# Performance work log

Measured on AMD Instinct MI355X. Metric: run time of the kernel, lower is better.

The kernel has to match this reference:

```python
import jax, jax.numpy as jnp
import numpy as np

# BERT-base dims; 768 and max_sent_num=64 come from the module/config.
N, S, V, D, L, H, F = 8, 512, 30522, 768, 12, 12, 3072
DH = D // H
MAX_SENT = 64
LN_EPS = 1e-12
SCALE = float(np.sqrt(DH))


def _ln(x, g, b):
    m = jnp.mean(x, axis=-1, keepdims=True)
    v = jnp.mean(jnp.square(x - m), axis=-1, keepdims=True)
    return (x - m) * jax.lax.rsqrt(v + LN_EPS) * g + b


def setup_inputs() -> dict:
    key = jax.random.key(0)
    ks = jax.random.split(key, 10)
    # random token ids in a range avoiding the special ids 102/103
    ids = jax.random.randint(ks[0], (N, S), 999, 30000, dtype=jnp.int32)
    # variable per-doc sentence region -> ragged number of [MASK](103) separators (8..64)
    cutoff = jax.random.randint(ks[1], (N, 1), 64, S + 1)
    pos = jnp.arange(S)[None, :]
    sent_pos = ((pos % 8) == 7) & (pos < cutoff)
    ids = jnp.where(sent_pos, 103, ids)
    ids = ids.at[:, 0].set(102)  # exactly one [SEP]=102 per doc (required by the slice-assign)
    amask = jnp.ones((N, S), dtype=jnp.int32)
    g = lambda k, shape: 0.02 * jax.random.normal(k, shape, dtype=jnp.float32)
    inp = dict(input_ids_bert=ids, attention_mask_bert=amask)
    inp["tok_emb"] = g(ks[2], (V, D))
    inp["pos_emb"] = g(ks[3], (S, D))
    inp["emb_ln_g"] = jnp.ones((D,), jnp.float32)
    inp["emb_ln_b"] = jnp.zeros((D,), jnp.float32)
    inp["Wqkv"] = g(ks[4], (L, D, 3 * D))
    inp["bqkv"] = jnp.zeros((L, 3 * D), jnp.float32)
    inp["Wo"] = g(ks[5], (L, D, D))
    inp["bo"] = jnp.zeros((L, D), jnp.float32)
    inp["ln1_g"] = jnp.ones((L, D), jnp.float32)
    inp["ln1_b"] = jnp.zeros((L, D), jnp.float32)
    inp["W1"] = g(ks[6], (L, D, F))
    inp["b1"] = jnp.zeros((L, F), jnp.float32)
    inp["W2"] = g(ks[7], (L, F, D))
    inp["b2"] = jnp.zeros((L, D), jnp.float32)
    inp["ln2_g"] = jnp.ones((L, D), jnp.float32)
    inp["ln2_b"] = jnp.zeros((L, D), jnp.float32)
    return inp


def _bert(ids, amask, tok_emb, pos_emb, emb_ln_g, emb_ln_b,
          Wqkv, bqkv, Wo, bo, ln1_g, ln1_b, W1, b1, W2, b2, ln2_g, ln2_b):
    x = tok_emb[ids] + pos_emb[None, :, :]            # [N,S,D]
    x = _ln(x, emb_ln_g, emb_ln_b)
    bias = (1.0 - amask[:, None, None, :].astype(x.dtype)) * -1e9  # [N,1,1,S]

    def layer(x, p):
        wqkv, bq, wo, bo_, g1, b1n, w1, b1f, w2, b2f, g2, b2n = p
        qkv = x @ wqkv + bq
        q, k, v = jnp.split(qkv, 3, axis=-1)
        q = q.reshape(N, S, H, DH)
        k = k.reshape(N, S, H, DH)
        v = v.reshape(N, S, H, DH)
        att = jnp.einsum('bqhd,bkhd->bhqk', q, k) / SCALE + bias
        att = jax.nn.softmax(att, axis=-1)
        o = jnp.einsum('bhqk,bkhd->bqhd', att, v).reshape(N, S, D)
        x2 = _ln(x + o @ wo + bo_, g1, b1n)
        h = jax.nn.gelu(x2 @ w1 + b1f, approximate=False)
        return _ln(x2 + h @ w2 + b2f, g2, b2n), None

    x, _ = jax.lax.scan(layer, x, (Wqkv, bqkv, Wo, bo, ln1_g, ln1_b, W1, b1, W2, b2, ln2_g, ln2_b))
    return x


def _gather_scatter(ids, h):
    # Vectorized form of the per-doc python loop:
    #   out[doc, :n_sent] = concat([cls_emb(102), sent_embs(103)])[:-1]
    mask_sent = ids == 103
    mask_cls = ids == 102
    n_cls = mask_cls.sum(axis=1, keepdims=True)              # == 1 per doc
    total_sent = mask_sent.sum(axis=1, keepdims=True)        # ragged count
    rank_sent = jnp.cumsum(mask_sent, axis=1) - 1
    rank_cls = jnp.cumsum(mask_cls, axis=1) - 1
    dest = jnp.where(mask_cls, rank_cls,
                     jnp.where(mask_sent, n_cls + rank_sent, MAX_SENT))
    valid = (mask_cls | mask_sent) & (dest < total_sent) & (dest < MAX_SENT)
    dest_safe = jnp.where(valid, dest, MAX_SENT)             # dump invalid into scratch row
    vals = jnp.where(valid[..., None], h, 0.0)
    out = jnp.zeros((ids.shape[0], MAX_SENT + 1, D), dtype=h.dtype)
    out = out.at[jnp.arange(ids.shape[0])[:, None], dest_safe].set(vals)
    return out[:, :MAX_SENT]


def reference(input_ids_bert, attention_mask_bert, tok_emb, pos_emb, emb_ln_g, emb_ln_b,
              Wqkv, bqkv, Wo, bo, ln1_g, ln1_b, W1, b1, W2, b2, ln2_g, ln2_b):
    h = _bert(input_ids_bert, attention_mask_bert, tok_emb, pos_emb, emb_ln_g, emb_ln_b,
              Wqkv, bqkv, Wo, bo, ln1_g, ln1_b, W1, b1, W2, b2, ln2_g, ln2_b)
    return _gather_scatter(input_ids_bert, h)
```

## Files before the change

### kernel.cpp

```cpp
#include <hip/hip_runtime.h>
#include <hip/hip_bf16.h>

#define DEV static __device__ __forceinline__

using short8 = __attribute__((ext_vector_type(8))) short;
using f32x4 = __attribute__((ext_vector_type(4))) float;

DEV short f2bf(float f) {
  union { float f; unsigned u; } x; x.f = f;
  unsigned r = x.u + 0x7fffu + ((x.u >> 16) & 1u);
  return (short)(r >> 16);
}

DEV float bf2f(short s) {
  union { unsigned u; float f; } x; x.u = ((unsigned)(unsigned short)s) << 16;
  return x.f;
}

DEV void gload16(const void* g, void* lds) {
  __builtin_amdgcn_global_load_lds(
      (const __attribute__((address_space(1))) void*)g,
      (__attribute__((address_space(3))) void*)lds, 16, 0, 0);
}

DEV float erf_fast(float x) {
  float ax = fabsf(x);
  float t = __fdividef(1.f, 1.f + 0.3275911f * ax);
  float y = t * (0.254829592f + t * (-0.284496736f +
            t * (1.421413741f + t * (-1.453152027f + t * 1.061405429f))));
  float r = 1.f - y * __expf(-ax * ax);
  return copysignf(r, x);
}

DEV void swz_grid(int& bx, int& by, int& bz) {
  const int nx = gridDim.x, ny = gridDim.y;
  const int nwg = nx * ny * (int)gridDim.z;
  const int lin = (int)blockIdx.x + nx * ((int)blockIdx.y + ny * (int)blockIdx.z);
  const int cpx = nwg >> 3;
  const int s = (lin & 7) * cpx + (lin >> 3);
  bx = s % nx;
  const int t = s / nx;
  by = t % ny;
  bz = t / ny;
}

DEV void transpose_tile(const float* in, short* out, int K, int N, int tt, int nt,
                        int tid, short (*t)[72]) {
  const int n0 = (tt % nt) * 64, k0 = (tt / nt) * 64;
  #pragma unroll
  for (int p = 0; p < 4; ++p) {
    int r = p * 16 + (tid >> 4), c4 = tid & 15;
    float4 v = *reinterpret_cast<const float4*>(in + (size_t)(k0 + r) * N + n0 + c4 * 4);
    t[r][c4 * 4 + 0] = f2bf(v.x);
    t[r][c4 * 4 + 1] = f2bf(v.y);
    t[r][c4 * 4 + 2] = f2bf(v.z);
    t[r][c4 * 4 + 3] = f2bf(v.w);
  }
  __syncthreads();
  #pragma unroll
  for (int q = 0; q < 2; ++q) {
    int n = tid >> 2, kc = (tid & 3) + q * 4;
    short8 o;
    #pragma unroll
    for (int j = 0; j < 8; ++j) o[j] = t[kc * 8 + j][n];
    *reinterpret_cast<short8*>(out + (size_t)(n0 + n) * K + k0 + kc * 8) = o;
  }
}

__global__ __launch_bounds__(256) void transpose_all_k(
    const float* __restrict__ Wqkv, const float* __restrict__ Wo,
    const float* __restrict__ W1, const float* __restrict__ W2,
    short* __restrict__ wqkvT, short* __restrict__ woT,
    short* __restrict__ w1T, short* __restrict__ w2T)
{
  __shared__ short t[64][72];
  const int b = blockIdx.x, tid = threadIdx.x;
  const float* in; short* out; int K, N, tt, nt;
  if (b < 432)       { in = Wqkv; out = wqkvT; K = 768;  N = 2304; tt = b;        nt = 36; }
  else if (b < 576)  { in = Wo;   out = woT;   K = 768;  N = 768;  tt = b - 432;  nt = 12; }
  else if (b < 1152) { in = W1;   out = w1T;   K = 768;  N = 3072; tt = b - 576;  nt = 48; }
  else               { in = W2;   out = w2T;   K = 3072; N = 768;  tt = b - 1152; nt = 12; }
  transpose_tile(in, out, K, N, tt, nt, tid, t);
}

__global__ __launch_bounds__(256) void transpose12_k(
    const float* __restrict__ Wqkv, const float* __restrict__ Wo,
    const float* __restrict__ W1, const float* __restrict__ W2,
    short* __restrict__ wqkvT, short* __restrict__ woT,
    short* __restrict__ w1T, short* __restrict__ w2T)
{
  __shared__ short t[64][72];
  const int b = blockIdx.x, l = blockIdx.z, tid = threadIdx.x;
  const float* in; short* out; int K, N, tt, nt;
  if (b < 432)       { in = Wqkv + (size_t)l * 768 * 2304; out = wqkvT + (size_t)l * 2304 * 768; K = 768;  N = 2304; tt = b;        nt = 36; }
  else if (b < 576)  { in = Wo   + (size_t)l * 768 * 768;  out = woT   + (size_t)l * 768 * 768;  K = 768;  N = 768;  tt = b - 432;  nt = 12; }
  else if (b < 1152) { in = W1   + (size_t)l * 768 * 3072; out = w1T   + (size_t)l * 3072 * 768; K = 768;  N = 3072; tt = b - 576;  nt = 48; }
  else               { in = W2   + (size_t)l * 3072 * 768; out = w2T   + (size_t)l * 768 * 3072; K = 3072; N = 768;  tt = b - 1152; nt = 12; }
  transpose_tile(in, out, K, N, tt, nt, tid, t);
}

template <int BM, int EPI>
__global__ __launch_bounds__(256) void gemm_bt(
    const short* __restrict__ A, const short* __restrict__ Bt,
    const float* __restrict__ bias, const float* __restrict__ resid,
    void* __restrict__ Cout, int M, int Nn, int K)
{
  constexpr int AW = BM / 64;
  constexpr int MI = BM / 32;
  __shared__ short As[2 * BM * 32];
  __shared__ short Bs[2 * 128 * 32];
  int bx, by, bz;
  swz_grid(bx, by, bz);
  const int tid = threadIdx.x, lane = tid & 63, w = tid >> 6;
  const int wr = w >> 1, wc = w & 1;
  const int l15 = lane & 15, l4 = lane >> 4;
  const int m0 = by * BM, n0 = bx * 128;
  const int crow = lane >> 2, ccol = (lane & 3) * 8;

  f32x4 acc[MI][4] = {};

  for (int k0 = 0; k0 < K; k0 += 64) {
    #pragma unroll
    for (int ks = 0; ks < 2; ++ks) {
      #pragma unroll
      for (int s = 0; s < AW; ++s) {
        int c = w * AW + s;
        gload16(A + (size_t)(m0 + c * 16 + crow) * K + k0 + ks * 32 + ccol,
                &As[ks * BM * 32 + c * 512]);
      }
      #pragma unroll
      for (int s = 0; s < 2; ++s) {
        int c = w * 2 + s;
        gload16(Bt + (size_t)(n0 + c * 16 + crow) * K + k0 + ks * 32 + ccol,
                &Bs[ks * 128 * 32 + c * 512]);
      }
    }
    __syncthreads();

    #pragma unroll
    for (int ks = 0; ks < 2; ++ks) {
      short8 af[MI], bfr[4];
      #pragma unroll
      for (int i = 0; i < MI; ++i)
        af[i] = *reinterpret_cast<const short8*>(
            &As[ks * BM * 32 + (wr * (BM / 2) + i * 16 + l15) * 32 + l4 * 8]);
      #pragma unroll
      for (int j = 0; j < 4; ++j)
        bfr[j] = *reinterpret_cast<const short8*>(
            &Bs[ks * 128 * 32 + (wc * 64 + j * 16 + l15) * 32 + l4 * 8]);
      #pragma unroll
      for (int i = 0; i < MI; ++i)
        #pragma unroll
        for (int j = 0; j < 4; ++j)
          acc[i][j] = __builtin_amdgcn_mfma_f32_16x16x32_bf16(af[i], bfr[j], acc[i][j], 0, 0, 0);
    }
    __syncthreads();
  }

  #pragma unroll
  for (int i = 0; i < MI; ++i) {
    #pragma unroll
    for (int j = 0; j < 4; ++j) {
      #pragma unroll
      for (int r = 0; r < 4; ++r) {
        int row = m0 + wr * (BM / 2) + i * 16 + l4 * 4 + r;
        int col = n0 + wc * 64 + j * 16 + l15;
        float v = acc[i][j][r] + bias[col];
        if constexpr (EPI == 1) v = 0.5f * v * (1.0f + erf_fast(v * 0.70710678118654752f));
        ((short*)Cout)[(size_t)row * Nn + col] = f2bf(v);
      }
    }
  }
}

__global__ __launch_bounds__(256) void gemm_sk(
    const short* __restrict__ A, const short* __restrict__ Bt,
    short* __restrict__ p0, short* __restrict__ p1,
    short* __restrict__ p2, short* __restrict__ p3,
    int M, int Nn, int Kstride, int Klen)
{
  __shared__ short As[2 * 128 * 32];
  __shared__ short Bs[2 * 128 * 32];
  int bx, by, bz;
  swz_grid(bx, by, bz);
  const int tid = threadIdx.x, lane = tid & 63, w = tid >> 6;
  const int wr = w >> 1, wc = w & 1;
  const int l15 = lane & 15, l4 = lane >> 4;
  const int m0 = by * 128, n0 = bx * 128;
  const int koff = bz * Klen;
  const int crow = lane >> 2, ccol = (lane & 3) * 8;

  f32x4 acc[4][4] = {};

  for (int k0 = 0; k0 < Klen; k0 += 64) {
    #pragma unroll
    for (int ks = 0; ks < 2; ++ks) {
      #pragma unroll
      for (int s = 0; s < 2; ++s) {
        int c = w * 2 + s;
        gload16(A + (size_t)(m0 + c * 16 + crow) * Kstride + koff + k0 + ks * 32 + ccol,
                &As[ks * 4096 + c * 512]);
      }
      #pragma unroll
      for (int s = 0; s < 2; ++s) {
        int c = w * 2 + s;
        gload16(Bt + (size_t)(n0 + c * 16 + crow) * Kstride + koff + k0 + ks * 32 + ccol,
                &Bs[ks * 4096 + c * 512]);
      }
    }
    __syncthreads();

    #pragma unroll
    for (int ks = 0; ks < 2; ++ks) {
      short8 af[4], bfr[4];
      #pragma unroll
      for (int i = 0; i < 4; ++i)
        af[i] = *reinterpret_cast<const short8*>(
            &As[ks * 4096 + (wr * 64 + i * 16 + l15) * 32 + l4 * 8]);
      #pragma unroll
      for (int j = 0; j < 4; ++j)
        bfr[j] = *reinterpret_cast<const short8*>(
            &Bs[ks * 4096 + (wc * 64 + j * 16 + l15) * 32 + l4 * 8]);
      #pragma unroll
      for (int i = 0; i < 4; ++i)
        #pragma unroll
        for (int j = 0; j < 4; ++j)
          acc[i][j] = __builtin_amdgcn_mfma_f32_16x16x32_bf16(af[i], bfr[j], acc[i][j], 0, 0, 0);
    }
    __syncthreads();
  }

  short* P = (bz == 0) ? p0 : (bz == 1) ? p1 : (bz == 2) ? p2 : p3;
  #pragma unroll
  for (int i = 0; i < 4; ++i)
    #pragma unroll
    for (int j = 0; j < 4; ++j)
      #pragma unroll
      for (int r = 0; r < 4; ++r) {
        int row = m0 + wr * 64 + i * 16 + l4 * 4 + r;
        int col = n0 + wc * 64 + j * 16 + l15;
        P[(size_t)row * Nn + col] = f2bf(acc[i][j][r]);
      }
}

__global__ __launch_bounds__(256) void attn_k(
    const short* __restrict__ qkv, const int* __restrict__ amask,
    short* __restrict__ out)
{
  __shared__ short Kl[64][72];
  __shared__ short Vt[64][68];
  __shared__ short Pl[4][16][72];
  int bx, by, bz;
  swz_grid(bx, by, bz);
  const int b = bz, h = by, qt = bx;
  const int tid = threadIdx.x, lane = tid & 63, w = tid >> 6;
  const int l15 = lane & 15, l4 = lane >> 4;
  const int tok0 = b * 512;
  const int q0 = qt * 64 + w * 16;

  short8 qf[2];
  #pragma unroll
  for (int kk = 0; kk < 2; ++kk)
    qf[kk] = *reinterpret_cast<const short8*>(
        qkv + (size_t)(tok0 + q0 + l15) * 2304 + h * 64 + kk * 32 + l4 * 8);

  f32x4 oacc[4] = {};
  float mrow[4], lrow[4];
  #pragma unroll
  for (int r = 0; r < 4; ++r) { mrow[r] = -1e30f; lrow[r] = 0.f; }

  for (int kt0 = 0; kt0 < 512; kt0 += 64) {
    #pragma unroll
    for (int i = 0; i < 2; ++i) {
      int c = tid + i * 256;
      int r = c >> 3, dc = c & 7;
      short8 v = *reinterpret_cast<const short8*>(
          qkv + (size_t)(tok0 + kt0 + r) * 2304 + 768 + h * 64 + dc * 8);
      *reinterpret_cast<short8*>(&Kl[r][dc * 8]) = v;
    }
    #pragma unroll
    for (int i = 0; i < 2; ++i) {
      int c = tid + i * 256;
      int r = c >> 3, dc = c & 7;
      short8 v = *reinterpret_cast<const short8*>(
          qkv + (size_t)(tok0 + kt0 + r) * 2304 + 1536 + h * 64 + dc * 8);
      #pragma unroll
      for (int j = 0; j < 8; ++j) Vt[dc * 8 + j][r] = v[j];
    }
    __syncthreads();

    f32x4 sacc[4] = {};
    #pragma unroll
    for (int t = 0; t < 4; ++t) {
      #pragma unroll
      for (int kk = 0; kk < 2; ++kk) {
        short8 kf = *reinterpret_cast<const short8*>(&Kl[t * 16 + l15][kk * 32 + l4 * 8]);
        sacc[t] = __builtin_amdgcn_mfma_f32_16x16x32_bf16(qf[kk], kf, sacc[t], 0, 0, 0);
      }
    }
    float p[4][4];
    #pragma unroll
    for (int t = 0; t < 4; ++t) {
      int ktok = kt0 + t * 16 + l15;
      float biasv = amask[b * 512 + ktok] ? 0.f : -1e9f;
      #pragma unroll
      for (int r = 0; r < 4; ++r) p[t][r] = sacc[t][r] * 0.125f + biasv;
    }
    #pragma unroll
    for (int r = 0; r < 4; ++r) {
      float mx = fmaxf(fmaxf(p[0][r], p[1][r]), fmaxf(p[2][r], p[3][r]));
      #pragma unroll
      for (int s = 1; s <= 8; s <<= 1) mx = fmaxf(mx, __shfl_xor(mx, s, 64));
      float mnew = fmaxf(mrow[r], mx);
      float alpha = __expf(mrow[r] - mnew);
      mrow[r] = mnew;
      float sum = 0.f;
      #pragma unroll
      for (int t = 0; t < 4; ++t) { p[t][r] = __expf(p[t][r] - mnew); sum += p[t][r]; }
      #pragma unroll
      for (int s = 1; s <= 8; s <<= 1) sum += __shfl_xor(sum, s, 64);
      lrow[r] = lrow[r] * alpha + sum;
      #pragma unroll
      for (int t = 0; t < 4; ++t) oacc[t][r] *= alpha;
    }
    #pragma unroll
    for (int t = 0; t < 4; ++t)
      #pragma unroll
      for (int r = 0; r < 4; ++r)
        Pl[w][l4 * 4 + r][t * 16 + l15] = f2bf(p[t][r]);
    #pragma unroll
    for (int kk = 0; kk < 2; ++kk) {
      short8 pf = *reinterpret_cast<const short8*>(&Pl[w][l15][kk * 32 + l4 * 8]);
      #pragma unroll
      for (int t = 0; t < 4; ++t) {
        const unsigned* vp = reinterpret_cast<const unsigned*>(&Vt[t * 16 + l15][0]);
        union { short8 s; unsigned u[4]; } vu;
        #pragma unroll
        for (int w2 = 0; w2 < 4; ++w2) vu.u[w2] = vp[kk * 16 + l4 * 4 + w2];
        oacc[t] = __builtin_amdgcn_mfma_f32_16x16x32_bf16(pf, vu.s, oacc[t], 0, 0, 0);
      }
    }
    __syncthreads();
  }

  #pragma unroll
  for (int t = 0; t < 4; ++t)
    #pragma unroll
    for (int r = 0; r < 4; ++r) {
      int tok = tok0 + q0 + l4 * 4 + r;
      int dh = t * 16 + l15;
      out[(size_t)tok * 768 + h * 64 + dh] = f2bf(oacc[t][r] / lrow[r]);
    }
}

__global__ __launch_bounds__(256) void ln2_k(
    const short* __restrict__ p0, const short* __restrict__ p1,
    const short* __restrict__ p2, const short* __restrict__ p3,
    const float* __restrict__ bias, const float* __restrict__ resid,
    const float* __restrict__ g, const float* __restrict__ be,
    float* __restrict__ xf, short* __restrict__ xb)
{
  const int t = blockIdx.x, tid = threadIdx.x;
  const size_t base = (size_t)t * 768;
  float v[3], s = 0.f, ss = 0.f;
  #pragma unroll
  for (int i = 0; i < 3; ++i) {
    int c = tid + i * 256;
    v[i] = (bf2f(p0[base + c]) + bf2f(p1[base + c]))
         + (bf2f(p2[base + c]) + bf2f(p3[base + c]))
         + bias[c] + resid[base + c];
    s += v[i]; ss += v[i] * v[i];
  }
  __shared__ float red[4][2];
  #pragma unroll
  for (int m = 1; m <= 32; m <<= 1) { s += __shfl_xor(s, m, 64); ss += __shfl_xor(ss, m, 64); }
  int w = tid >> 6;
  if ((tid & 63) == 0) { red[w][0] = s; red[w][1] = ss; }
  __syncthreads();
  s = red[0][0] + red[1][0] + red[2][0] + red[3][0];
  ss = red[0][1] + red[1][1] + red[2][1] + red[3][1];
  float mean = s * (1.f / 768.f);
  float var = ss * (1.f / 768.f) - mean * mean;
  float rs = rsqrtf(var + 1e-12f);
  #pragma unroll
  for (int i = 0; i < 3; ++i) {
    int c = tid + i * 256;
    float o = (v[i] - mean) * rs * g[c] + be[c];
    xf[base + c] = o;
    xb[base + c] = f2bf(o);
  }
}

__global__ __launch_bounds__(256) void embed_ln_k(
    const int* __restrict__ ids, const float* __restrict__ tok_emb,
    const float* __restrict__ pos_emb, const float* __restrict__ g,
    const float* __restrict__ be, float* __restrict__ xf, short* __restrict__ xb)
{
  const int t = blockIdx.x, tid = threadIdx.x;
  const int id = ids[t], sp = t & 511;
  float v[3], s = 0.f, ss = 0.f;
  #pragma unroll
  for (int i = 0; i < 3; ++i) {
    int c = tid + i * 256;
    v[i] = tok_emb[(size_t)id * 768 + c] + pos_emb[(size_t)sp * 768 + c];
    s += v[i]; ss += v[i] * v[i];
  }
  __shared__ float red[4][2];
  #pragma unroll
  for (int m = 1; m <= 32; m <<= 1) { s += __shfl_xor(s, m, 64); ss += __shfl_xor(ss, m, 64); }
  int w = tid >> 6;
  if ((tid & 63) == 0) { red[w][0] = s; red[w][1] = ss; }
  __syncthreads();
  s = red[0][0] + red[1][0] + red[2][0] + red[3][0];
  ss = red[0][1] + red[1][1] + red[2][1] + red[3][1];
  float mean = s * (1.f / 768.f);
  float var = ss * (1.f / 768.f) - mean * mean;
  float rs = rsqrtf(var + 1e-12f);
  #pragma unroll
  for (int i = 0; i < 3; ++i) {
    int c = tid + i * 256;
    float o = (v[i] - mean) * rs * g[c] + be[c];
    xf[(size_t)t * 768 + c] = o;
    xb[(size_t)t * 768 + c] = f2bf(o);
  }
}

__global__ __launch_bounds__(512) void gather_k(
    const int* __restrict__ ids, const float* __restrict__ x, float* __restrict__ out)
{
  const int doc = blockIdx.x, tid = threadIdx.x;
  const int lane = tid & 63, w = tid >> 6;
  __shared__ int src[64];
  __shared__ int wave_sent[8];
  __shared__ int cls_pos;
  if (tid < 64) src[tid] = -1;
  if (tid == 0) cls_pos = 0x7fffffff;
  __syncthreads();

  const int id = ids[doc * 512 + tid];
  const bool is_sent = (id == 103);
  const unsigned long long m = __ballot(is_sent);
  if (lane == 0) wave_sent[w] = __popcll(m);
  if (id == 102) atomicMin(&cls_pos, tid);
  __syncthreads();

  int total = 0, prefix = 0;
  #pragma unroll
  for (int i = 0; i < 8; ++i) {
    int c = wave_sent[i];
    if (i < w) prefix += c;
    total += c;
  }
  if (is_sent) {
    unsigned long long lt = lane ? (~0ULL >> (64 - lane)) : 0ULL;
    int d = 1 + prefix + __popcll(m & lt);
    if (d < total && d < 64) src[d] = tid;
  }
  if (tid == 0 && total > 0 && cls_pos != 0x7fffffff) src[0] = cls_pos;
  __syncthreads();

  for (int i = tid; i < 64 * 192; i += 512) {
    int row = i / 192, c4 = i - row * 192;
    int sp = src[row];
    float4 v = make_float4(0.f, 0.f, 0.f, 0.f);
    if (sp >= 0)
      v = reinterpret_cast<const float4*>(x + (size_t)(doc * 512 + sp) * 768)[c4];
    reinterpret_cast<float4*>(out + (size_t)doc * 64 * 768)[i] = v;
  }
}

extern "C" void kernel_launch(void* const* d_in, const int* in_sizes, int n_in,
                              void* d_out, int out_size, void* d_ws, size_t ws_size,
                              hipStream_t stream)
{
  const int* ids = (const int*)d_in[0];
  const int* am = (const int*)d_in[1];
  const float* tok_emb = (const float*)d_in[2];
  const float* pos_emb = (const float*)d_in[3];
  const float* eg = (const float*)d_in[4];
  const float* eb = (const float*)d_in[5];
  const float* Wqkv = (const float*)d_in[6];
  const float* bqkv = (const float*)d_in[7];
  const float* Wo = (const float*)d_in[8];
  const float* bo = (const float*)d_in[9];
  const float* g1 = (const float*)d_in[10];
  const float* b1n = (const float*)d_in[11];
  const float* W1 = (const float*)d_in[12];
  const float* b1f = (const float*)d_in[13];
  const float* W2 = (const float*)d_in[14];
  const float* b2f = (const float*)d_in[15];
  const float* g2 = (const float*)d_in[16];
  const float* b2n = (const float*)d_in[17];

  char* ws = (char*)d_ws;
  float* x_f   = (float*)(ws);
  short* x_b   = (short*)(ws + 12582912);
  float* x2_f  = (float*)(ws + 18874368);
  short* x2_b  = (short*)(ws + 31457280);
  short* pp0   = (short*)(ws + 37748736);
  short* pp1   = (short*)(ws + 37748736 + 6291456);
  short* qkv   = (short*)(ws + 50331648);
  short* pp2   = (short*)(ws + 50331648);
  short* pp3   = (short*)(ws + 50331648 + 6291456);
  short* attn  = (short*)(ws + 69206016);
  short* hb    = (short*)(ws + 75497472);
  const size_t WQ = 2304ull * 768, WO = 768ull * 768, W1S = 3072ull * 768, W2S = 768ull * 3072;
  const size_t NEED_ALL = 100663296ull + 12ull * (WQ + WO + W1S + W2S) * 2ull;
  const bool big = ws_size >= NEED_ALL;

  short* wqkvT = (short*)(ws + 100663296);
  short* woT, *w1T, *w2T;
  if (big) {
    woT = wqkvT + 12 * WQ;
    w1T = woT + 12 * WO;
    w2T = w1T + 12 * W1S;
  } else {
    woT = (short*)(ws + 104202240);
    w1T = (short*)(ws + 105381888);
    w2T = (short*)(ws + 110100480);
  }

  embed_ln_k<<<4096, 256, 0, stream>>>(ids, tok_emb, pos_emb, eg, eb, x_f, x_b);

  if (big)
    transpose12_k<<<dim3(1728, 1, 12), 256, 0, stream>>>(
        Wqkv, Wo, W1, W2, wqkvT, woT, w1T, w2T);

  for (int l = 0; l < 12; ++l) {
    short *wq, *wo, *w1, *w2;
    if (big) {
      wq = wqkvT + l * WQ; wo = woT + l * WO; w1 = w1T + l * W1S; w2 = w2T + l * W2S;
    } else {
      transpose_all_k<<<1728, 256, 0, stream>>>(
          Wqkv + (size_t)l * 768 * 2304, Wo + (size_t)l * 768 * 768,
          W1 + (size_t)l * 768 * 3072, W2 + (size_t)l * 3072 * 768,
          wqkvT, woT, w1T, w2T);
      wq = wqkvT; wo = woT; w1 = w1T; w2 = w2T;
    }

    gemm_bt<128, 0><<<dim3(18, 32), 256, 0, stream>>>(
        x_b, wq, bqkv + (size_t)l * 2304, nullptr, qkv, 4096, 2304, 768);
    attn_k<<<dim3(8, 12, 8), 256, 0, stream>>>(qkv, am, attn);

    gemm_sk<<<dim3(6, 32, 4), 256, 0, stream>>>(
        attn, wo, pp0, pp1, pp2, pp3, 4096, 768, 768, 192);
    ln2_k<<<4096, 256, 0, stream>>>(
        pp0, pp1, pp2, pp3, bo + (size_t)l * 768, x_f,
        g1 + (size_t)l * 768, b1n + (size_t)l * 768, x2_f, x2_b);

    gemm_bt<128, 1><<<dim3(24, 32), 256, 0, stream>>>(
        x2_b, w1, b1f + (size_t)l * 3072, nullptr, hb, 4096, 3072, 768);

    gemm_sk<<<dim3(6, 32, 4), 256, 0, stream>>>(
        hb, w2, pp0, pp1, pp2, pp3, 4096, 768, 3072, 768);
    ln2_k<<<4096, 256, 0, stream>>>(
        pp0, pp1, pp2, pp3, b2f + (size_t)l * 768, x2_f,
        g2 + (size_t)l * 768, b2n + (size_t)l * 768, x_f, x_b);
  }

  gather_k<<<8, 512, 0, stream>>>(ids, x_f, (float*)d_out);
}
```

Baseline: 2.240 ms.

## Double attention KV tile to 128 keys and drop grid swizzle

The attention kernel now processes 128 keys per iteration instead of 64, with larger LDS buffers for K, transposed V and P. This halves the number of barrier-separated tile loads and online-softmax rescales per query block. Separately, the XCD-aware block swizzle is removed from all GEMM and attention kernels in favour of plain blockIdx mapping, which may reduce L2 locality across chiplets. The larger tiles also raise register and LDS use, which could lower occupancy.

```diff
diff --git a/kernel.cpp b/kernel.cpp
--- a/kernel.cpp
+++ b/kernel.cpp
@@ -30,18 +30,6 @@
             t * (1.421413741f + t * (-1.453152027f + t * 1.061405429f))));
   float r = 1.f - y * __expf(-ax * ax);
   return copysignf(r, x);
-}
-
-DEV void swz_grid(int& bx, int& by, int& bz) {
-  const int nx = gridDim.x, ny = gridDim.y;
-  const int nwg = nx * ny * (int)gridDim.z;
-  const int lin = (int)blockIdx.x + nx * ((int)blockIdx.y + ny * (int)blockIdx.z);
-  const int cpx = nwg >> 3;
-  const int s = (lin & 7) * cpx + (lin >> 3);
-  bx = s % nx;
-  const int t = s / nx;
-  by = t % ny;
-  bz = t / ny;
 }
 
 DEV void transpose_tile(const float* in, short* out, int K, int N, int tt, int nt,
@@ -109,12 +97,10 @@
   constexpr int MI = BM / 32;
   __shared__ short As[2 * BM * 32];
   __shared__ short Bs[2 * 128 * 32];
-  int bx, by, bz;
-  swz_grid(bx, by, bz);
   const int tid = threadIdx.x, lane = tid & 63, w = tid >> 6;
   const int wr = w >> 1, wc = w & 1;
   const int l15 = lane & 15, l4 = lane >> 4;
-  const int m0 = by * BM, n0 = bx * 128;
+  const int m0 = blockIdx.y * BM, n0 = blockIdx.x * 128;
   const int crow = lane >> 2, ccol = (lane & 3) * 8;
 
   f32x4 acc[MI][4] = {};
@@ -181,13 +167,11 @@
 {
   __shared__ short As[2 * 128 * 32];
   __shared__ short Bs[2 * 128 * 32];
-  int bx, by, bz;
-  swz_grid(bx, by, bz);
   const int tid = threadIdx.x, lane = tid & 63, w = tid >> 6;
   const int wr = w >> 1, wc = w & 1;
   const int l15 = lane & 15, l4 = lane >> 4;
-  const int m0 = by * 128, n0 = bx * 128;
-  const int koff = bz * Klen;
+  const int m0 = blockIdx.y * 128, n0 = blockIdx.x * 128;
+  const int koff = blockIdx.z * Klen;
   const int crow = lane >> 2, ccol = (lane & 3) * 8;
 
   f32x4 acc[4][4] = {};
@@ -230,7 +214,7 @@
     __syncthreads();
   }
 
-  short* P = (bz == 0) ? p0 : (bz == 1) ? p1 : (bz == 2) ? p2 : p3;
+  short* P = (blockIdx.z == 0) ? p0 : (blockIdx.z == 1) ? p1 : (blockIdx.z == 2) ? p2 : p3;
   #pragma unroll
   for (int i = 0; i < 4; ++i)
     #pragma unroll
@@ -247,12 +231,10 @@
     const short* __restrict__ qkv, const int* __restrict__ amask,
     short* __restrict__ out)
 {
-  __shared__ short Kl[64][72];
-  __shared__ short Vt[64][68];
-  __shared__ short Pl[4][16][72];
-  int bx, by, bz;
-  swz_grid(bx, by, bz);
-  const int b = bz, h = by, qt = bx;
+  __shared__ short Kl[128][72];
+  __shared__ short Vt[64][132];
+  __shared__ short Pl[4][16][136];
+  const int b = blockIdx.z, h = blockIdx.y, qt = blockIdx.x;
   const int tid = threadIdx.x, lane = tid & 63, w = tid >> 6;
   const int l15 = lane & 15, l4 = lane >> 4;
   const int tok0 = b * 512;
@@ -269,9 +251,9 @@
   #pragma unroll
   for (int r = 0; r < 4; ++r) { mrow[r] = -1e30f; lrow[r] = 0.f; }
 
-  for (int kt0 = 0; kt0 < 512; kt0 += 64) {
-    #pragma unroll
-    for (int i = 0; i < 2; ++i) {
+  for (int kt0 = 0; kt0 < 512; kt0 += 128) {
+    #pragma unroll
+    for (int i = 0; i < 4; ++i) {
       int c = tid + i * 256;
       int r = c >> 3, dc = c & 7;
       short8 v = *reinterpret_cast<const short8*>(
@@ -279,7 +261,7 @@
       *reinterpret_cast<short8*>(&Kl[r][dc * 8]) = v;
     }
     #pragma unroll
-    for (int i = 0; i < 2; ++i) {
+    for (int i = 0; i < 4; ++i) {
       int c = tid + i * 256;
       int r = c >> 3, dc = c & 7;
       short8 v = *reinterpret_cast<const short8*>(
@@ -289,18 +271,18 @@
     }
     __syncthreads();
 
-    f32x4 sacc[4] = {};
-    #pragma unroll
-    for (int t = 0; t < 4; ++t) {
+    f32x4 sacc[8] = {};
+    #pragma unroll
+    for (int t = 0; t < 8; ++t) {
       #pragma unroll
       for (int kk = 0; kk < 2; ++kk) {
         short8 kf = *reinterpret_cast<const short8*>(&Kl[t * 16 + l15][kk * 32 + l4 * 8]);
         sacc[t] = __builtin_amdgcn_mfma_f32_16x16x32_bf16(qf[kk], kf, sacc[t], 0, 0, 0);
       }
     }
-    float p[4][4];
-    #pragma unroll
-    for (int t = 0; t < 4; ++t) {
+    float p[8][4];
+    #pragma unroll
+    for (int t = 0; t < 8; ++t) {
       int ktok = kt0 + t * 16 + l15;
       float biasv = amask[b * 512 + ktok] ? 0.f : -1e9f;
       #pragma unroll
@@ -308,7 +290,9 @@
     }
     #pragma unroll
     for (int r = 0; r < 4; ++r) {
-      float mx = fmaxf(fmaxf(p[0][r], p[1][r]), fmaxf(p[2][r], p[3][r]));
+      float mx = p[0][r];
+      #pragma unroll
+      for (int t = 1; t < 8; ++t) mx = fmaxf(mx, p[t][r]);
       #pragma unroll
       for (int s = 1; s <= 8; s <<= 1) mx = fmaxf(mx, __shfl_xor(mx, s, 64));
       float mnew = fmaxf(mrow[r], mx);
@@ -316,7 +300,7 @@
       mrow[r] = mnew;
       float sum = 0.f;
       #pragma unroll
-      for (int t = 0; t < 4; ++t) { p[t][r] = __expf(p[t][r] - mnew); sum += p[t][r]; }
+      for (int t = 0; t < 8; ++t) { p[t][r] = __expf(p[t][r] - mnew); sum += p[t][r]; }
       #pragma unroll
       for (int s = 1; s <= 8; s <<= 1) sum += __shfl_xor(sum, s, 64);
       lrow[r] = lrow[r] * alpha + sum;
@@ -324,12 +308,12 @@
       for (int t = 0; t < 4; ++t) oacc[t][r] *= alpha;
     }
     #pragma unroll
-    for (int t = 0; t < 4; ++t)
+    for (int t = 0; t < 8; ++t)
       #pragma unroll
       for (int r = 0; r < 4; ++r)
         Pl[w][l4 * 4 + r][t * 16 + l15] = f2bf(p[t][r]);
     #pragma unroll
-    for (int kk = 0; kk < 2; ++kk) {
+    for (int kk = 0; kk < 4; ++kk) {
       short8 pf = *reinterpret_cast<const short8*>(&Pl[w][l15][kk * 32 + l4 * 8]);
       #pragma unroll
       for (int t = 0; t < 4; ++t) {
```

After: 2.368 ms. 1.06x slower.
